# Performance work log

Hardware: AMD Instinct MI355X
Metric: run time of the kernel (lower is better)

## Reference

```python
import jax, jax.numpy as jnp
import numpy as np

NPOINTS = 1024


def setup_inputs() -> dict:
    key = jax.random.key(0)
    B, N, C = 64, 131072, 3
    pos = jax.random.normal(key, (B, N, C), dtype=jnp.float32)
    return {"pos": pos, "start_idx": 0}


def reference(pos, start_idx):
    """Farthest point sampling. pos: (B, N, C) -> indices (B, NPOINTS) int32."""
    B, N, C = pos.shape
    start = jnp.full((B,), start_idx, dtype=jnp.int32)
    dist0 = jnp.full((B, N), jnp.inf, dtype=pos.dtype)

    def step(carry, _):
        dist, last = carry                                   # dist: (B,N), last: (B,)
        last_pos = jnp.take_along_axis(pos, last[:, None, None], axis=1)  # (B,1,C)
        d = jnp.sum((pos - last_pos) ** 2, axis=-1)          # (B,N) squared dist to newest sample
        dist = jnp.minimum(dist, d)                          # min to-sample-set distance
        nxt = jnp.argmax(dist, axis=-1).astype(jnp.int32)    # farthest point
        return (dist, nxt), last                             # emit index selected this step

    (_, _), idxs = jax.lax.scan(step, (dist0, start), None, length=NPOINTS)
    return idxs.T  # (B, NPOINTS); first column == start_idx
```

## Files before the change

### kernel.cpp

```cpp
#include <hip/hip_runtime.h>
#include <stdint.h>

#define NB    64
#define NN    131072
#define NPTS  1024
#define WPB   4
#define TPB   1024
#define NWAVE (TPB / 64)
#define CHUNK (NN / WPB)
#define PPT   (CHUNK / TPB)
#define RPTS  20
#define LPTS  12
#define RPAIR (RPTS / 2)
#define LPAIR (LPTS / 2)

typedef float v2f __attribute__((ext_vector_type(2)));
typedef unsigned long long u64;

static __device__ __forceinline__ v2f vmin2(v2f a, v2f b) {
#if __has_builtin(__builtin_elementwise_min)
    return __builtin_elementwise_min(a, b);
#else
    v2f r; r.x = fminf(a.x, b.x); r.y = fminf(a.y, b.y); return r;
#endif
}


__global__ __launch_bounds__(TPB)
__attribute__((amdgpu_waves_per_eu(4, 4)))
void fps_kernel(
    const float* __restrict__ pos,
    const int*   __restrict__ start_p,
    int*         __restrict__ out,
    u64*         __restrict__ slots)
{
#pragma clang fp contract(off)
    const int wg   = blockIdx.x;
    const int xcd  = wg & 7;
    const int sl   = wg >> 3;
    const int b    = xcd * 8 + (sl >> 2);
    const int r    = sl & 3;
    const int t    = threadIdx.x;
    const int lane = t & 63;
    const int wv   = t >> 6;

    const float* __restrict__ P  = pos + (size_t)b * NN * 3;
    const float* __restrict__ Pc = P + (size_t)r * CHUNK * 3;
    u64* __restrict__ bslots = slots + (size_t)b * NPTS * WPB;

    __shared__ float lx[LPAIR * TPB * 2];
    __shared__ float ly[LPAIR * TPB * 2];
    __shared__ float lz[LPAIR * TPB * 2];
    __shared__ u64   wred[2][NWAVE];

    v2f rx[RPAIR], ry[RPAIR], rz[RPAIR];
#pragma unroll
    for (int p = 0; p < RPAIR; ++p) {
        const float* a = Pc + (size_t)(t + (2 * p) * TPB) * 3;
        const float* c = a + (size_t)TPB * 3;
        rx[p] = (v2f){a[0], c[0]};
        ry[p] = (v2f){a[1], c[1]};
        rz[p] = (v2f){a[2], c[2]};
    }
#pragma unroll
    for (int l = 0; l < LPAIR; ++l) {
        const float* a = Pc + (size_t)(t + (RPTS + 2 * l) * TPB) * 3;
        const float* c = a + (size_t)TPB * 3;
        const int idx = (l * TPB + t) * 2;
        lx[idx] = a[0]; lx[idx + 1] = c[0];
        ly[idx] = a[1]; ly[idx + 1] = c[1];
        lz[idx] = a[2]; lz[idx + 1] = c[2];
    }

    const int start = start_p[0];
    float sx = P[(size_t)start * 3 + 0];
    float sy = P[(size_t)start * 3 + 1];
    float sz = P[(size_t)start * 3 + 2];
    if (r == 0 && t == 0) out[(size_t)b * NPTS] = start;

    v2f dist[PPT / 2];
#pragma unroll
    for (int p = 0; p < PPT / 2; ++p)
        dist[p] = (v2f){__builtin_inff(), __builtin_inff()};

    const int gbase = r * CHUNK;

    for (int k = 1; k < NPTS; ++k) {
        const int bank = k & 1;
        const v2f s0 = (v2f){sx, sx}, s1 = (v2f){sy, sy}, s2 = (v2f){sz, sz};
        float best = -1.0f;
        int   bi   = 0;

#define PAIR_STEP(DP, PX, PY, PZ, I0)                                    \
        {                                                                \
            v2f dx = (PX) - s0, dy = (PY) - s1, dz = (PZ) - s2;          \
            v2f d  = (dx * dx + dy * dy) + dz * dz;                      \
            v2f nd = vmin2(dist[DP], d);                                 \
            dist[DP] = nd;                                               \
            if (nd.x > best) { best = nd.x; bi = (I0); }                 \
            if (nd.y > best) { best = nd.y; bi = (I0) + TPB; }           \
        }

#pragma unroll
        for (int p = 0; p < RPAIR; ++p)
            PAIR_STEP(p, rx[p], ry[p], rz[p], gbase + t + (2 * p) * TPB);
#pragma unroll
        for (int l = 0; l < LPAIR; ++l) {
            const int idx = (l * TPB + t) * 2;
            v2f px = *reinterpret_cast<const v2f*>(&lx[idx]);
            v2f py = *reinterpret_cast<const v2f*>(&ly[idx]);
            v2f pz = *reinterpret_cast<const v2f*>(&lz[idx]);
            PAIR_STEP(RPAIR + l, px, py, pz, gbase + t + (RPTS + 2 * l) * TPB);
        }
#undef PAIR_STEP

        u64 pk = ((u64)__float_as_uint(best) << 32) | (unsigned)~bi;

#pragma unroll
        for (int o = 32; o >= 1; o >>= 1) {
            u64 q = __shfl_xor(pk, o, 64);
            if (q > pk) pk = q;
        }
        if (lane == 0) wred[bank][wv] = pk;
        __syncthreads();

        u64 v = wred[bank][lane & (NWAVE - 1)];
#pragma unroll
        for (int o = 1; o < NWAVE; o <<= 1) {
            u64 q = __shfl_xor(v, o, 64);
            if (q > v) v = q;
        }
        if (t == 0)
            __hip_atomic_store(&bslots[(size_t)k * WPB + r], v,
                               __ATOMIC_RELAXED, __HIP_MEMORY_SCOPE_AGENT);

        const u64* sp = &bslots[(size_t)k * WPB + (lane & 3)];
        u64 g;
        for (;;) {
            g = __hip_atomic_load(sp, __ATOMIC_RELAXED, __HIP_MEMORY_SCOPE_AGENT);
            if (g) break;
            __builtin_amdgcn_s_sleep(1);
        }
#pragma unroll
        for (int o = 1; o <= 2; o <<= 1) {
            u64 q = __shfl_xor(g, o, 64);
            if (q > g) g = q;
        }
        const int widx = (int)~(unsigned)g;
        if (r == 0 && t == 0) out[(size_t)b * NPTS + k] = widx;
        sx = P[(size_t)widx * 3 + 0];
        sy = P[(size_t)widx * 3 + 1];
        sz = P[(size_t)widx * 3 + 2];
    }
}

extern "C" void kernel_launch(void* const* d_in, const int* in_sizes, int n_in,
                              void* d_out, int out_size, void* d_ws, size_t ws_size,
                              hipStream_t stream)
{
    const float* pos     = (const float*)d_in[0];
    const int*   start_p = (const int*)d_in[1];
    int*         out     = (int*)d_out;
    u64*         slots   = (u64*)d_ws;

    hipMemsetAsync(d_ws, 0, (size_t)NB * NPTS * WPB * sizeof(u64), stream);

    void* args[] = { (void*)&pos, (void*)&start_p, (void*)&out, (void*)&slots };
    hipError_t e = hipLaunchCooperativeKernel((const void*)fps_kernel,
                                              dim3(NB * WPB), dim3(TPB),
                                              args, 0, stream);
    if (e != hipSuccess) {
        fps_kernel<<<dim3(NB * WPB), dim3(TPB), 0, stream>>>(pos, start_p, out, slots);
    }
}
```

Baseline: 4.274 ms.

## Template FPS kernel and split each batch across 8 workgroups of 512 threads

The kernel becomes a template over block size, workgroups per batch, and register/LDS point counts. When the workspace is large enough, each batch is split over 8 workgroups of 512 threads (512 blocks total, two per CU via launch_bounds) instead of 4 workgroups of 1024. This uses more of the CUs and shrinks per-block reductions, at the cost of a wider cross-workgroup slot reduction per step and more spin-wait traffic. The change also drops the waves_per_eu attribute, which may alter register allocation.

```diff
diff --git a/kernel.cpp b/kernel.cpp
--- a/kernel.cpp
+++ b/kernel.cpp
@@ -4,15 +4,6 @@
 #define NB    64
 #define NN    131072
 #define NPTS  1024
-#define WPB   4
-#define TPB   1024
-#define NWAVE (TPB / 64)
-#define CHUNK (NN / WPB)
-#define PPT   (CHUNK / TPB)
-#define RPTS  20
-#define LPTS  12
-#define RPAIR (RPTS / 2)
-#define LPAIR (LPTS / 2)
 
 typedef float v2f __attribute__((ext_vector_type(2)));
 typedef unsigned long long u64;
@@ -26,47 +17,53 @@
 }
 
 
-__global__ __launch_bounds__(TPB)
-__attribute__((amdgpu_waves_per_eu(4, 4)))
-void fps_kernel(
+template <int TPB_, int WPB_, int RPTS_, int LPTS_>
+__global__ __launch_bounds__(TPB_, 2) void fps_kernel(
     const float* __restrict__ pos,
     const int*   __restrict__ start_p,
     int*         __restrict__ out,
     u64*         __restrict__ slots)
 {
 #pragma clang fp contract(off)
+    constexpr int NWAVE = TPB_ / 64;
+    constexpr int CHUNK = NN / WPB_;
+    constexpr int PPT   = CHUNK / TPB_;
+    constexpr int RPAIR = RPTS_ / 2;
+    constexpr int LPAIR = LPTS_ / 2;
+    constexpr int WSH   = (WPB_ == 8) ? 3 : 2;
+
     const int wg   = blockIdx.x;
     const int xcd  = wg & 7;
     const int sl   = wg >> 3;
-    const int b    = xcd * 8 + (sl >> 2);
-    const int r    = sl & 3;
+    const int b    = xcd * 8 + (sl >> WSH);
+    const int r    = sl & (WPB_ - 1);
     const int t    = threadIdx.x;
     const int lane = t & 63;
     const int wv   = t >> 6;
 
     const float* __restrict__ P  = pos + (size_t)b * NN * 3;
     const float* __restrict__ Pc = P + (size_t)r * CHUNK * 3;
-    u64* __restrict__ bslots = slots + (size_t)b * NPTS * WPB;
+    u64* __restrict__ bslots = slots + (size_t)b * NPTS * WPB_;
 
-    __shared__ float lx[LPAIR * TPB * 2];
-    __shared__ float ly[LPAIR * TPB * 2];
-    __shared__ float lz[LPAIR * TPB * 2];
+    __shared__ float lx[LPAIR * TPB_ * 2];
+    __shared__ float ly[LPAIR * TPB_ * 2];
+    __shared__ float lz[LPAIR * TPB_ * 2];
     __shared__ u64   wred[2][NWAVE];
 
     v2f rx[RPAIR], ry[RPAIR], rz[RPAIR];
 #pragma unroll
     for (int p = 0; p < RPAIR; ++p) {
-        const float* a = Pc + (size_t)(t + (2 * p) * TPB) * 3;
-        const float* c = a + (size_t)TPB * 3;
+        const float* a = Pc + (size_t)(t + (2 * p) * TPB_) * 3;
+        const float* c = a + (size_t)TPB_ * 3;
         rx[p] = (v2f){a[0], c[0]};
         ry[p] = (v2f){a[1], c[1]};
         rz[p] = (v2f){a[2], c[2]};
     }
 #pragma unroll
     for (int l = 0; l < LPAIR; ++l) {
-        const float* a = Pc + (size_t)(t + (RPTS + 2 * l) * TPB) * 3;
-        const float* c = a + (size_t)TPB * 3;
-        const int idx = (l * TPB + t) * 2;
+        const float* a = Pc + (size_t)(t + (RPTS_ + 2 * l) * TPB_) * 3;
+        const float* c = a + (size_t)TPB_ * 3;
+        const int idx = (l * TPB_ + t) * 2;
         lx[idx] = a[0]; lx[idx + 1] = c[0];
         ly[idx] = a[1]; ly[idx + 1] = c[1];
         lz[idx] = a[2]; lz[idx + 1] = c[2];
@@ -98,19 +95,19 @@
             v2f nd = vmin2(dist[DP], d);                                 \
             dist[DP] = nd;                                               \
             if (nd.x > best) { best = nd.x; bi = (I0); }                 \
-            if (nd.y > best) { best = nd.y; bi = (I0) + TPB; }           \
+            if (nd.y > best) { best = nd.y; bi = (I0) + TPB_; }          \
         }
 
 #pragma unroll
         for (int p = 0; p < RPAIR; ++p)
-            PAIR_STEP(p, rx[p], ry[p], rz[p], gbase + t + (2 * p) * TPB);
+            PAIR_STEP(p, rx[p], ry[p], rz[p], gbase + t + (2 * p) * TPB_);
 #pragma unroll
         for (int l = 0; l < LPAIR; ++l) {
-            const int idx = (l * TPB + t) * 2;
+            const int idx = (l * TPB_ + t) * 2;
             v2f px = *reinterpret_cast<const v2f*>(&lx[idx]);
             v2f py = *reinterpret_cast<const v2f*>(&ly[idx]);
             v2f pz = *reinterpret_cast<const v2f*>(&lz[idx]);
-            PAIR_STEP(RPAIR + l, px, py, pz, gbase + t + (RPTS + 2 * l) * TPB);
+            PAIR_STEP(RPAIR + l, px, py, pz, gbase + t + (RPTS_ + 2 * l) * TPB_);
         }
 #undef PAIR_STEP
 
@@ -131,10 +128,10 @@
             if (q > v) v = q;
         }
         if (t == 0)
-            __hip_atomic_store(&bslots[(size_t)k * WPB + r], v,
+            __hip_atomic_store(&bslots[(size_t)k * WPB_ + r], v,
                                __ATOMIC_RELAXED, __HIP_MEMORY_SCOPE_AGENT);
 
-        const u64* sp = &bslots[(size_t)k * WPB + (lane & 3)];
+        const u64* sp = &bslots[(size_t)k * WPB_ + (lane & (WPB_ - 1))];
         u64 g;
         for (;;) {
             g = __hip_atomic_load(sp, __ATOMIC_RELAXED, __HIP_MEMORY_SCOPE_AGENT);
@@ -142,7 +139,7 @@
             __builtin_amdgcn_s_sleep(1);
         }
 #pragma unroll
-        for (int o = 1; o <= 2; o <<= 1) {
+        for (int o = 1; o < WPB_; o <<= 1) {
             u64 q = __shfl_xor(g, o, 64);
             if (q > g) g = q;
         }
@@ -163,13 +160,26 @@
     int*         out     = (int*)d_out;
     u64*         slots   = (u64*)d_ws;
 
-    hipMemsetAsync(d_ws, 0, (size_t)NB * NPTS * WPB * sizeof(u64), stream);
+    const size_t need8 = (size_t)NB * NPTS * 8 * sizeof(u64);
+    const size_t need4 = (size_t)NB * NPTS * 4 * sizeof(u64);
 
-    void* args[] = { (void*)&pos, (void*)&start_p, (void*)&out, (void*)&slots };
-    hipError_t e = hipLaunchCooperativeKernel((const void*)fps_kernel,
-                                              dim3(NB * WPB), dim3(TPB),
-                                              args, 0, stream);
-    if (e != hipSuccess) {
-        fps_kernel<<<dim3(NB * WPB), dim3(TPB), 0, stream>>>(pos, start_p, out, slots);
+    if (ws_size >= need8) {
+        hipMemsetAsync(d_ws, 0, need8, stream);
+        void* args[] = { (void*)&pos, (void*)&start_p, (void*)&out, (void*)&slots };
+        hipError_t e = hipLaunchCooperativeKernel(
+            (const void*)fps_kernel<512, 8, 24, 8>,
+            dim3(NB * 8), dim3(512), args, 0, stream);
+        if (e != hipSuccess)
+            fps_kernel<512, 8, 24, 8><<<dim3(NB * 8), dim3(512), 0, stream>>>(
+                pos, start_p, out, slots);
+    } else {
+        hipMemsetAsync(d_ws, 0, need4, stream);
+        void* args[] = { (void*)&pos, (void*)&start_p, (void*)&out, (void*)&slots };
+        hipError_t e = hipLaunchCooperativeKernel(
+            (const void*)fps_kernel<1024, 4, 20, 12>,
+            dim3(NB * 4), dim3(1024), args, 0, stream);
+        if (e != hipSuccess)
+            fps_kernel<1024, 4, 20, 12><<<dim3(NB * 4), dim3(1024), 0, stream>>>(
+                pos, start_p, out, slots);
     }
 }
```

Measured after the change: 5.746 ms. 1.34x slower.
